# Kernel optimization log

Measured on AMD Instinct MI355X. Metric: run time of the kernel, lower is better.

## Reference

```python
import jax, jax.numpy as jnp
import numpy as np

EPS_ATTN = 1e-6
LN_EPS = 1e-5

def _layernorm(x, g, b):
    mu = jnp.mean(x, axis=-1, keepdims=True)
    var = jnp.var(x, axis=-1, keepdims=True)
    return (x - mu) * jax.lax.rsqrt(var + LN_EPS) * g + b

def _phi(x):
    return jax.nn.elu(x) + 1.0

def setup_inputs() -> dict:
    key = jax.random.key(0)
    ks = jax.random.split(key, 8)
    B, T, D, H = 2, 4096, 128, 128  # D = token_dim = d+1, H = hidden_dim
    s = 0.02
    return {
        "tokens": jax.random.normal(ks[0], (B, T, D), dtype=jnp.float32),
        "Wq": jax.random.normal(ks[1], (D, H), dtype=jnp.float32) * s,
        "Wk": jax.random.normal(ks[2], (D, H), dtype=jnp.float32) * s,
        "Wv": jax.random.normal(ks[3], (D, D), dtype=jnp.float32) * s,
        "Wg": jax.random.normal(ks[4], (D, D), dtype=jnp.float32) * s,
        "bg": jnp.zeros((D,), dtype=jnp.float32),
        "Wo": jax.random.normal(ks[5], (D, D), dtype=jnp.float32) * s,
        "g1": jnp.ones((D,), dtype=jnp.float32),
        "b1": jnp.zeros((D,), dtype=jnp.float32),
        "g2": jnp.ones((D,), dtype=jnp.float32),
        "b2": jnp.zeros((D,), dtype=jnp.float32),
    }

def reference(tokens, Wq, Wk, Wv, Wg, bg, Wo, g1, b1, g2, b2):
    x = _layernorm(tokens, g1, b1)                 # (b,t,m)
    Q = x @ Wq                                     # (b,t,h)
    K = x @ Wk                                     # (b,t,h)
    V = x @ Wv                                     # (b,t,m)
    G = jax.nn.sigmoid(x @ Wg + bg)                # (b,t,m)
    Vg = V * G
    Qp = _phi(Q)
    Kp = _phi(K)
    # causal linear attention via cumulative outer products
    kv = jnp.einsum('bth,btm->bthm', Kp, Vg)       # (b,t,h,m)
    S_kv = jnp.cumsum(kv, axis=1)
    S_k = jnp.cumsum(Kp, axis=1)
    numerator = jnp.einsum('bth,bthm->btm', Qp, S_kv)
    denom = jnp.maximum(jnp.einsum('bth,bth->bt', Qp, S_k), EPS_ATTN)
    attn_out = numerator / denom[..., None]
    out = tokens + (attn_out @ Wo) * 0.1
    return _layernorm(out, g2, b2)
```

## Files before the change

kernel.cpp:

```cpp
#include <hip/hip_runtime.h>
#include <math.h>

#define T_ 4096
#define D_ 128
#define NTOK 8192
#define CHUNK 64
#define NCB 64
#define NCH 128
#define LN_EPS 1e-5f
#define EPS_ATTN 1e-6f

typedef __attribute__((ext_vector_type(8))) short bf16x8;
typedef __attribute__((ext_vector_type(4))) short bf16x4;
typedef __attribute__((ext_vector_type(2))) short bf16x2;
typedef __attribute__((ext_vector_type(4))) float f32x4;

__device__ inline short f2bf(float f) {
  unsigned u = __builtin_bit_cast(unsigned, f);
  u += 0x7fffu + ((u >> 16) & 1u);
  return (short)(u >> 16);
}
__device__ inline float bf2f(short s) {
  unsigned u = ((unsigned)(unsigned short)s) << 16;
  return __builtin_bit_cast(float, u);
}
__device__ inline float phi_(float x) { return x > 0.f ? x + 1.f : __expf(x); }

__global__ __launch_bounds__(256) void k_wprep(const float* __restrict__ Wq,
    const float* __restrict__ Wk, const float* __restrict__ Wv,
    const float* __restrict__ Wg, const float* __restrict__ Wo,
    short* __restrict__ WT) {
  const float* W = blockIdx.x==0?Wq: blockIdx.x==1?Wk: blockIdx.x==2?Wv: blockIdx.x==3?Wg:Wo;
  short* out = WT + blockIdx.x*D_*D_;
  __shared__ float lds[128][132];
  const int tid = threadIdx.x;
  #pragma unroll
  for (int it = 0; it < 16; ++it) {
    const int f = it*1024 + tid*4;
    const int k = f >> 7, n = f & 127;
    const float4 v = *(const float4*)&W[f];
    lds[k][n] = v.x; lds[k][n+1] = v.y; lds[k][n+2] = v.z; lds[k][n+3] = v.w;
  }
  __syncthreads();
  #pragma unroll
  for (int it = 0; it < 16; ++it) {
    const int f = it*1024 + tid*4;
    const int n = f >> 7, k = f & 127;
    bf16x4 o;
    o.x = f2bf(lds[k][n]);   o.y = f2bf(lds[k+1][n]);
    o.z = f2bf(lds[k+2][n]); o.w = f2bf(lds[k+3][n]);
    *(bf16x4*)&out[f] = o;
  }
}

__global__ __launch_bounds__(256) void k_qkvg(const float* __restrict__ tokens,
    const short* __restrict__ WT,
    const float* __restrict__ g1, const float* __restrict__ b1,
    const float* __restrict__ bg,
    short* __restrict__ Qp, short* __restrict__ Kp, short* __restrict__ KpT,
    short* __restrict__ VgT) {
  const int m0 = blockIdx.x * 32;
  const int y = blockIdx.y;
  const int tid = threadIdx.x;
  const int w = tid >> 6, l = tid & 63;
  __shared__ short xs[32][136];
  __shared__ short wsd[128][136];

  {
    const float2 gg = *(const float2*)&g1[l*2];
    const float2 bb = *(const float2*)&b1[l*2];
    float2 tv[8];
    #pragma unroll
    for (int it = 0; it < 8; ++it)
      tv[it] = *(const float2*)&tokens[(m0 + w*8 + it)*D_ + l*2];
    #pragma unroll
    for (int it = 0; it < 8; ++it) {
      const float2 v = tv[it];
      float s = v.x + v.y, qq = v.x*v.x + v.y*v.y;
      #pragma unroll
      for (int off = 1; off < 64; off <<= 1) {
        s += __shfl_xor(s, off); qq += __shfl_xor(qq, off);
      }
      const float mean = s*(1.f/D_);
      const float r2 = rsqrtf(qq*(1.f/D_) - mean*mean + LN_EPS);
      bf16x2 o;
      o.x = f2bf((v.x-mean)*r2*gg.x + bb.x);
      o.y = f2bf((v.y-mean)*r2*gg.y + bb.y);
      *(bf16x2*)&xs[w*8 + it][l*2] = o;
    }
  }

  auto stageW = [&](const short* __restrict__ Wb) {
    for (int v = tid; v < 2048; v += 256) {
      const int n = v >> 4, c8 = (v & 15)*8;
      *(bf16x8*)&wsd[n][c8] = *(const bf16x8*)&Wb[n*D_ + c8];
    }
  };

  const int i = l & 15, q = l >> 4;
  auto gemm = [&](f32x4 (*acc)[2]) {
    #pragma unroll
    for (int kk = 0; kk < 4; ++kk) {
      bf16x8 a[2], bfr[2];
      #pragma unroll
      for (int mt = 0; mt < 2; ++mt) a[mt] = *(const bf16x8*)&xs[mt*16+i][kk*32+q*8];
      #pragma unroll
      for (int nt = 0; nt < 2; ++nt) bfr[nt] = *(const bf16x8*)&wsd[w*32+nt*16+i][kk*32+q*8];
      #pragma unroll
      for (int mt = 0; mt < 2; ++mt)
        #pragma unroll
        for (int nt = 0; nt < 2; ++nt)
          acc[mt][nt] = __builtin_amdgcn_mfma_f32_16x16x32_bf16(a[mt], bfr[nt], acc[mt][nt], 0, 0, 0);
    }
  };

  stageW(WT + (y == 2 ? 2 : y)*D_*D_);
  __syncthreads();
  f32x4 acc[2][2];
  #pragma unroll
  for (int mt = 0; mt < 2; ++mt)
    #pragma unroll
    for (int nt = 0; nt < 2; ++nt) acc[mt][nt] = (f32x4){0.f,0.f,0.f,0.f};
  gemm(acc);

  if (y == 0) {
    #pragma unroll
    for (int mt = 0; mt < 2; ++mt)
      #pragma unroll
      for (int nt = 0; nt < 2; ++nt) {
        const int h = w*32 + nt*16 + i;
        #pragma unroll
        for (int r = 0; r < 4; ++r)
          Qp[(m0 + mt*16 + 4*q + r)*D_ + h] = f2bf(phi_(acc[mt][nt][r]));
      }
  } else if (y == 1) {
    #pragma unroll
    for (int mt = 0; mt < 2; ++mt)
      #pragma unroll
      for (int nt = 0; nt < 2; ++nt) {
        const int h = w*32 + nt*16 + i;
        const int t0 = m0 + mt*16 + 4*q;
        bf16x4 o;
        #pragma unroll
        for (int r = 0; r < 4; ++r) {
          const short bv = f2bf(phi_(acc[mt][nt][r]));
          Kp[(t0+r)*D_ + h] = bv;
          o[r] = bv;
        }
        *(bf16x4*)&KpT[h*NTOK + t0] = o;
      }
  } else {
    __syncthreads();
    stageW(WT + 3*D_*D_);
    __syncthreads();
    f32x4 accg[2][2];
    #pragma unroll
    for (int mt = 0; mt < 2; ++mt)
      #pragma unroll
      for (int nt = 0; nt < 2; ++nt) accg[mt][nt] = (f32x4){0.f,0.f,0.f,0.f};
    gemm(accg);
    #pragma unroll
    for (int mt = 0; mt < 2; ++mt)
      #pragma unroll
      for (int nt = 0; nt < 2; ++nt) {
        const int h = w*32 + nt*16 + i;
        const int t0 = m0 + mt*16 + 4*q;
        const float bgd = bg[h];
        bf16x4 o;
        #pragma unroll
        for (int r = 0; r < 4; ++r) {
          const float gv = 1.f/(1.f + __expf(-(accg[mt][nt][r] + bgd)));
          o[r] = f2bf(acc[mt][nt][r] * gv);
        }
        *(bf16x4*)&VgT[h*NTOK + t0] = o;
      }
  }
}

__global__ __launch_bounds__(256) void k_chunkkv(const short* __restrict__ KpT,
    const short* __restrict__ VgT,
    float* __restrict__ KVT, float* __restrict__ Ksum) {
  const int c = blockIdx.x, hh = blockIdx.y, dh = blockIdx.z;
  const int tid = threadIdx.x;
  const int tb = c*CHUNK;
  __shared__ short vgl[64][72];
  __shared__ short kpl[64][72];
  __shared__ float ksp[64][5];
  for (int u = tid; u < 512; u += 256) {
    const int dd = u >> 3, c8 = (u & 7)*8;
    *(bf16x8*)&vgl[dd][c8] = *(const bf16x8*)&VgT[(dh*64+dd)*NTOK + tb + c8];
    *(bf16x8*)&kpl[dd][c8] = *(const bf16x8*)&KpT[(hh*64+dd)*NTOK + tb + c8];
  }
  __syncthreads();
  const int w = tid >> 6, l = tid & 63, i = l & 15, q = l >> 4;
  f32x4 acc[4];
  #pragma unroll
  for (int nt = 0; nt < 4; ++nt) acc[nt] = (f32x4){0.f,0.f,0.f,0.f};
  #pragma unroll
  for (int kk = 0; kk < 2; ++kk) {
    bf16x8 a = *(const bf16x8*)&vgl[w*16+i][kk*32+q*8];
    #pragma unroll
    for (int nt = 0; nt < 4; ++nt) {
      bf16x8 bb = *(const bf16x8*)&kpl[nt*16+i][kk*32+q*8];
      acc[nt] = __builtin_amdgcn_mfma_f32_16x16x32_bf16(a, bb, acc[nt], 0, 0, 0);
    }
  }
  float* KVc = KVT + (size_t)c*16384;
  #pragma unroll
  for (int nt = 0; nt < 4; ++nt)
    #pragma unroll
    for (int r = 0; r < 4; ++r) {
      const int d = dh*64 + w*16 + 4*q + r;
      const int h = hh*64 + nt*16 + i;
      KVc[d*D_ + h] = acc[nt][r];
    }
  if (dh == 0) {
    const int h = tid >> 2, part = tid & 3;
    float s = 0.f;
    #pragma unroll
    for (int t = 0; t < 16; ++t) s += bf2f(kpl[h][part*16 + t]);
    ksp[h][part] = s;
    __syncthreads();
    if (tid < 64)
      Ksum[c*D_ + hh*64 + tid] = ksp[tid][0]+ksp[tid][1]+ksp[tid][2]+ksp[tid][3];
  }
}

__global__ __launch_bounds__(256) void k_prescore(const float* __restrict__ KVT,
    short* __restrict__ KVTb, float* __restrict__ Ksum,
    const short* __restrict__ Qp, const short* __restrict__ Kp,
    short* __restrict__ A, float* __restrict__ rowsum) {
  const int tid = threadIdx.x;
  if (blockIdx.x < 128) {
    const int b = blockIdx.x >> 6;
    const int e = (blockIdx.x & 63)*256 + tid;
    const size_t base = (size_t)b*NCB*16384 + e;
    float run = 0.f;
    #pragma unroll 8
    for (int c = 0; c < NCB; ++c) {
      const float v = KVT[base + (size_t)c*16384];
      KVTb[base + (size_t)c*16384] = f2bf(run);
      run += v;
    }
    return;
  }
  if (blockIdx.x == 128) {
    const int b = tid >> 7, h = tid & 127;
    float run = 0.f;
    #pragma unroll 8
    for (int c = 0; c < NCB; ++c) {
      const int idx = (b*NCB + c)*128 + h;
      const float v = Ksum[idx];
      Ksum[idx] = run;
      run += v;
    }
    return;
  }
  const int c = blockIdx.x - 129;
  const int tb = c*CHUNK;
  __shared__ short qpl[64][136], kpl[64][136];
  #pragma unroll
  for (int u = tid; u < 1024; u += 256) {
    const int t = u >> 4, c8 = (u & 15)*8;
    *(bf16x8*)&qpl[t][c8] = *(const bf16x8*)&Qp[(tb+t)*D_ + c8];
    *(bf16x8*)&kpl[t][c8] = *(const bf16x8*)&Kp[(tb+t)*D_ + c8];
  }
  __syncthreads();
  const int w = tid >> 6, l = tid & 63, i = l & 15, q = l >> 4;
  f32x4 acc[4];
  #pragma unroll
  for (int nt = 0; nt < 4; ++nt) acc[nt] = (f32x4){0.f,0.f,0.f,0.f};
  #pragma unroll
  for (int kk = 0; kk < 4; ++kk) {
    bf16x8 a = *(const bf16x8*)&qpl[w*16+i][kk*32+q*8];
    for (int nt = 0; nt <= w; ++nt) {
      bf16x8 bb = *(const bf16x8*)&kpl[nt*16+i][kk*32+q*8];
      acc[nt] = __builtin_amdgcn_mfma_f32_16x16x32_bf16(a, bb, acc[nt], 0, 0, 0);
    }
  }
  short* Ac = A + c*4096;
  float rs[4] = {0.f,0.f,0.f,0.f};
  #pragma unroll
  for (int nt = 0; nt < 4; ++nt) {
    #pragma unroll
    for (int r = 0; r < 4; ++r) {
      const int t = w*16 + 4*q + r;
      const int s = nt*16 + i;
      const float v = (nt <= w && s <= t) ? acc[nt][r] : 0.f;
      rs[r] += v;
      Ac[t*64 + s] = f2bf(v);
    }
  }
  #pragma unroll
  for (int r = 0; r < 4; ++r) {
    #pragma unroll
    for (int off = 1; off < 16; off <<= 1) rs[r] += __shfl_xor(rs[r], off);
  }
  if (i == 0) {
    #pragma unroll
    for (int r = 0; r < 4; ++r) rowsum[c*64 + w*16 + 4*q + r] = rs[r];
  }
}

__global__ __launch_bounds__(256) void k_attnout(const short* __restrict__ Aintra,
    const short* __restrict__ Qp, const short* __restrict__ VgT,
    const short* __restrict__ KVTb, const float* __restrict__ Ksum,
    const float* __restrict__ rowsum, short* __restrict__ attn) {
  const int c = blockIdx.x, dq = blockIdx.y, tid = threadIdx.x;
  const int tb = c*CHUNK;
  __shared__ short at[64][200], bt[32][200];
  __shared__ float ksl[128], dpart[64][4], denl[64];
  const short* Ac = Aintra + c*4096;
  #pragma unroll
  for (int u = tid; u < 512; u += 256) {
    const int t = u >> 3, c8 = (u & 7)*8;
    *(bf16x8*)&at[t][c8] = *(const bf16x8*)&Ac[t*64 + c8];
  }
  #pragma unroll
  for (int u = tid; u < 1024; u += 256) {
    const int t = u >> 4, c8 = (u & 15)*8;
    *(bf16x8*)&at[t][64 + c8] = *(const bf16x8*)&Qp[(tb+t)*D_ + c8];
  }
  for (int u = tid; u < 256; u += 256) {
    const int dd = u >> 3, c8 = (u & 7)*8;
    *(bf16x8*)&bt[dd][c8] = *(const bf16x8*)&VgT[(dq*32+dd)*NTOK + tb + c8];
  }
  #pragma unroll
  for (int u = tid; u < 512; u += 256) {
    const int dd = u >> 4, c8 = (u & 15)*8;
    *(bf16x8*)&bt[dd][64 + c8] = *(const bf16x8*)&KVTb[(size_t)c*16384 + (dq*32+dd)*D_ + c8];
  }
  if (tid < 128) ksl[tid] = Ksum[c*128 + tid];
  __syncthreads();
  {
    const int t = tid >> 2, part = tid & 3;
    float dot = 0.f;
    #pragma unroll
    for (int h = 0; h < 32; ++h) dot += bf2f(at[t][64 + part*32 + h]) * ksl[part*32 + h];
    dpart[t][part] = dot;
  }
  __syncthreads();
  if (tid < 64)
    denl[tid] = fmaxf(rowsum[c*64 + tid] + dpart[tid][0]+dpart[tid][1]+dpart[tid][2]+dpart[tid][3], EPS_ATTN);
  __syncthreads();
  const int w = tid >> 6, l = tid & 63, i = l & 15, q = l >> 4;
  f32x4 acc[2];
  #pragma unroll
  for (int nt = 0; nt < 2; ++nt) acc[nt] = (f32x4){0.f,0.f,0.f,0.f};
  #pragma unroll
  for (int kk = 0; kk < 6; ++kk) {
    bf16x8 a = *(const bf16x8*)&at[w*16+i][kk*32+q*8];
    #pragma unroll
    for (int nt = 0; nt < 2; ++nt) {
      bf16x8 bb = *(const bf16x8*)&bt[nt*16+i][kk*32+q*8];
      acc[nt] = __builtin_amdgcn_mfma_f32_16x16x32_bf16(a, bb, acc[nt], 0, 0, 0);
    }
  }
  #pragma unroll
  for (int r = 0; r < 4; ++r) {
    const int t = w*16 + 4*q + r;
    const float inv = 1.f / denl[t];
    #pragma unroll
    for (int nt = 0; nt < 2; ++nt)
      attn[(size_t)(tb+t)*D_ + dq*32 + nt*16 + i] = f2bf(acc[nt][r] * inv);
  }
}

__global__ __launch_bounds__(256) void k_outln2(const short* __restrict__ attn,
    const short* __restrict__ WoT, const float* __restrict__ tokens,
    const float* __restrict__ g2, const float* __restrict__ b2,
    float* __restrict__ out) {
  const int m0 = blockIdx.x*16, tid = threadIdx.x;
  __shared__ short al[16][136], wl[128][136];
  __shared__ float tl[16][132];
  __shared__ float suml[16][4], ssql[16][4];
  __shared__ float meanl[16], rstdl[16];
  __shared__ float gl[128], bl2[128];
  for (int u = tid; u < 256; u += 256) {
    const int t = u >> 4, c8 = (u & 15)*8;
    *(bf16x8*)&al[t][c8] = *(const bf16x8*)&attn[(m0+t)*D_ + c8];
  }
  #pragma unroll
  for (int u = tid; u < 2048; u += 256) {
    const int n = u >> 4, c8 = (u & 15)*8;
    *(bf16x8*)&wl[n][c8] = *(const bf16x8*)&WoT[n*D_ + c8];
  }
  #pragma unroll
  for (int u = tid; u < 512; u += 256) {
    const int t = u >> 5, c4 = (u & 31)*4;
    *(float4*)&tl[t][c4] = *(const float4*)&tokens[(m0+t)*D_ + c4];
  }
  if (tid < 128) { gl[tid] = g2[tid]; bl2[tid] = b2[tid]; }
  __syncthreads();
  const int w = tid >> 6, l = tid & 63, i = l & 15, q = l >> 4;
  f32x4 acc[2];
  #pragma unroll
  for (int j = 0; j < 2; ++j) acc[j] = (f32x4){0.f,0.f,0.f,0.f};
  #pragma unroll
  for (int kk = 0; kk < 4; ++kk) {
    bf16x8 a = *(const bf16x8*)&al[i][kk*32+q*8];
    #pragma unroll
    for (int j = 0; j < 2; ++j) {
      bf16x8 bb = *(const bf16x8*)&wl[(w*2+j)*16+i][kk*32+q*8];
      acc[j] = __builtin_amdgcn_mfma_f32_16x16x32_bf16(a, bb, acc[j], 0, 0, 0);
    }
  }
  float p[4][2], ps[4], qs[4];
  #pragma unroll
  for (int r = 0; r < 4; ++r) {
    const int t = 4*q + r;
    ps[r] = 0.f; qs[r] = 0.f;
    #pragma unroll
    for (int j = 0; j < 2; ++j) {
      const int col = w*32 + j*16 + i;
      const float v = tl[t][col] + 0.1f*acc[j][r];
      p[r][j] = v; ps[r] += v; qs[r] += v*v;
    }
  }
  #pragma unroll
  for (int r = 0; r < 4; ++r) {
    #pragma unroll
    for (int off = 1; off < 16; off <<= 1) {
      ps[r] += __shfl_xor(ps[r], off);
      qs[r] += __shfl_xor(qs[r], off);
    }
  }
  if (i == 0) {
    #pragma unroll
    for (int r = 0; r < 4; ++r) {
      suml[4*q+r][w] = ps[r];
      ssql[4*q+r][w] = qs[r];
    }
  }
  __syncthreads();
  if (tid < 16) {
    const float s = suml[tid][0]+suml[tid][1]+suml[tid][2]+suml[tid][3];
    const float qq = ssql[tid][0]+ssql[tid][1]+ssql[tid][2]+ssql[tid][3];
    const float mean = s*(1.f/D_);
    meanl[tid] = mean;
    rstdl[tid] = rsqrtf(qq*(1.f/D_) - mean*mean + LN_EPS);
  }
  __syncthreads();
  #pragma unroll
  for (int r = 0; r < 4; ++r) {
    const int t = 4*q + r;
    const float mean = meanl[t], rr = rstdl[t];
    #pragma unroll
    for (int j = 0; j < 2; ++j) {
      const int col = w*32 + j*16 + i;
      out[(m0+t)*D_ + col] = (p[r][j]-mean)*rr*gl[col] + bl2[col];
    }
  }
}

extern "C" void kernel_launch(void* const* d_in, const int* in_sizes, int n_in,
                              void* d_out, int out_size, void* d_ws, size_t ws_size,
                              hipStream_t stream) {
  const float* tokens = (const float*)d_in[0];
  const float* Wq = (const float*)d_in[1];
  const float* Wk = (const float*)d_in[2];
  const float* Wv = (const float*)d_in[3];
  const float* Wg = (const float*)d_in[4];
  const float* bg = (const float*)d_in[5];
  const float* Wo = (const float*)d_in[6];
  const float* g1 = (const float*)d_in[7];
  const float* b1 = (const float*)d_in[8];
  const float* g2 = (const float*)d_in[9];
  const float* b2 = (const float*)d_in[10];

  char* base = (char*)d_ws;
  short* Qp     = (short*)(base);
  short* Kp     = (short*)(base + (2u<<20));
  short* KpT    = (short*)(base + (4u<<20));
  short* VgT    = (short*)(base + (6u<<20));
  short* attn   = (short*)(base + (8u<<20));
  short* KVTb   = (short*)(base + (10u<<20));
  short* Aintra = (short*)(base + (14u<<20));
  short* WT     = (short*)(base + (15u<<20));
  float* rowsum = (float*)(base + (15u<<20) + (256u<<10));
  float* Ksum   = (float*)(base + (15u<<20) + (512u<<10));
  float* KVT    = (float*)(base + (16u<<20));

  short* WoT = WT + 4*D_*D_;

  k_wprep<<<5, 256, 0, stream>>>(Wq, Wk, Wv, Wg, Wo, WT);
  k_qkvg<<<dim3(NTOK/32, 3), 256, 0, stream>>>(tokens, WT, g1, b1, bg,
                                               Qp, Kp, KpT, VgT);
  k_chunkkv<<<dim3(NCH, 2, 2), 256, 0, stream>>>(KpT, VgT, KVT, Ksum);
  k_prescore<<<257, 256, 0, stream>>>(KVT, KVTb, Ksum, Qp, Kp, Aintra, rowsum);
  k_attnout<<<dim3(NCH, 4), 256, 0, stream>>>(Aintra, Qp, VgT, KVTb, Ksum, rowsum, attn);
  k_outln2<<<NTOK/16, 256, 0, stream>>>(attn, WoT, tokens, g2, b2, (float*)d_out);
}
```

Before: 114.5 us.

## Fuse all stages into one cooperative persistent kernel with grid syncs

Replaces the six separate kernel launches with a single cooperative kernel of 512 blocks that separates the stages with grid-wide syncs. The aim is to remove launch gaps and per-kernel ramp-up and tail costs. Work is also rebalanced across blocks: weight prep is split over 10 blocks, Q and K blocks each handle two row tiles, and the score and chunk-KV stages share one phase. The risks are the cost of the grid barriers and lower occupancy from the large static shared-memory buffer and the 2-blocks-per-CU launch bound.

Result: slower. 413.6 us (+261.3%).

```diff
diff --git a/kernel.cpp b/kernel.cpp
--- a/kernel.cpp
+++ b/kernel.cpp
@@ -1,7 +1,9 @@
 #include <hip/hip_runtime.h>
+#include <hip/hip_cooperative_groups.h>
 #include <math.h>
 
-#define T_ 4096
+namespace cg = cooperative_groups;
+
 #define D_ 128
 #define NTOK 8192
 #define CHUNK 64
@@ -9,6 +11,7 @@
 #define NCH 128
 #define LN_EPS 1e-5f
 #define EPS_ATTN 1e-6f
+#define NBLK 512
 
 typedef __attribute__((ext_vector_type(8))) short bf16x8;
 typedef __attribute__((ext_vector_type(4))) short bf16x4;
@@ -26,430 +29,477 @@
 }
 __device__ inline float phi_(float x) { return x > 0.f ? x + 1.f : __expf(x); }
 
-__global__ __launch_bounds__(256) void k_wprep(const float* __restrict__ Wq,
-    const float* __restrict__ Wk, const float* __restrict__ Wv,
-    const float* __restrict__ Wg, const float* __restrict__ Wo,
-    short* __restrict__ WT) {
-  const float* W = blockIdx.x==0?Wq: blockIdx.x==1?Wk: blockIdx.x==2?Wv: blockIdx.x==3?Wg:Wo;
-  short* out = WT + blockIdx.x*D_*D_;
-  __shared__ float lds[128][132];
+__global__ __launch_bounds__(256, 2) void k_mega(
+    const float* __restrict__ tokens,
+    const float* __restrict__ Wq, const float* __restrict__ Wk,
+    const float* __restrict__ Wv, const float* __restrict__ Wg,
+    const float* __restrict__ bgp, const float* __restrict__ Wo,
+    const float* __restrict__ g1, const float* __restrict__ b1,
+    const float* __restrict__ g2, const float* __restrict__ b2,
+    float* __restrict__ out, char* __restrict__ ws)
+{
+  cg::grid_group grid = cg::this_grid();
   const int tid = threadIdx.x;
-  #pragma unroll
-  for (int it = 0; it < 16; ++it) {
-    const int f = it*1024 + tid*4;
-    const int k = f >> 7, n = f & 127;
-    const float4 v = *(const float4*)&W[f];
-    lds[k][n] = v.x; lds[k][n+1] = v.y; lds[k][n+2] = v.z; lds[k][n+3] = v.w;
+  const int bid = blockIdx.x;
+
+  short* Qp     = (short*)(ws);
+  short* Kp     = (short*)(ws + (2u<<20));
+  short* KpT    = (short*)(ws + (4u<<20));
+  short* VgT    = (short*)(ws + (6u<<20));
+  short* attnb  = (short*)(ws + (8u<<20));
+  short* KVTb   = (short*)(ws + (10u<<20));
+  short* Aintra = (short*)(ws + (14u<<20));
+  short* WT     = (short*)(ws + (15u<<20));
+  float* rowsum = (float*)(ws + (15u<<20) + (256u<<10));
+  float* Ksum   = (float*)(ws + (15u<<20) + (512u<<10));
+  float* KVT    = (float*)(ws + (16u<<20));
+
+  __shared__ __align__(16) char smem[62720];
+
+  const int w = tid >> 6, l = tid & 63;
+  const int i = l & 15, q = l >> 4;
+
+  if (bid < 10) {
+    const int mat = bid >> 1, half = bid & 1;
+    const float* W = mat==0?Wq: mat==1?Wk: mat==2?Wv: mat==3?Wg:Wo;
+    short* o = WT + mat*D_*D_;
+    float (*lds)[132] = (float(*)[132])smem;
+    #pragma unroll
+    for (int it = 0; it < 8; ++it) {
+      const int f = it*1024 + tid*4;
+      const int kk = f >> 7, n = f & 127;
+      const float4 v = *(const float4*)&W[(half*64 + kk)*D_ + n];
+      lds[kk][n] = v.x; lds[kk][n+1] = v.y; lds[kk][n+2] = v.z; lds[kk][n+3] = v.w;
+    }
+    __syncthreads();
+    #pragma unroll
+    for (int it = 0; it < 8; ++it) {
+      const int f = it*1024 + tid*4;
+      const int n = f >> 6, kl = f & 63;
+      bf16x4 ov;
+      ov.x = f2bf(lds[kl][n]);   ov.y = f2bf(lds[kl+1][n]);
+      ov.z = f2bf(lds[kl+2][n]); ov.w = f2bf(lds[kl+3][n]);
+      *(bf16x4*)&o[n*D_ + half*64 + kl] = ov;
+    }
   }
-  __syncthreads();
-  #pragma unroll
-  for (int it = 0; it < 16; ++it) {
-    const int f = it*1024 + tid*4;
-    const int n = f >> 7, k = f & 127;
-    bf16x4 o;
-    o.x = f2bf(lds[k][n]);   o.y = f2bf(lds[k+1][n]);
-    o.z = f2bf(lds[k+2][n]); o.w = f2bf(lds[k+3][n]);
-    *(bf16x4*)&out[f] = o;
+  grid.sync();
+
+  {
+    short (*xs)[136]  = (short(*)[136])smem;
+    short (*wsd)[136] = (short(*)[136])(smem + 8704);
+
+    auto stageW = [&](const short* __restrict__ Wb) {
+      for (int v = tid; v < 2048; v += 256) {
+        const int n = v >> 4, c8 = (v & 15)*8;
+        *(bf16x8*)&wsd[n][c8] = *(const bf16x8*)&Wb[n*D_ + c8];
+      }
+    };
+    auto doLN = [&](int m0) {
+      const float2 gg = *(const float2*)&g1[l*2];
+      const float2 bb = *(const float2*)&b1[l*2];
+      float2 tv[8];
+      #pragma unroll
+      for (int it = 0; it < 8; ++it)
+        tv[it] = *(const float2*)&tokens[(m0 + w*8 + it)*D_ + l*2];
+      #pragma unroll
+      for (int it = 0; it < 8; ++it) {
+        const float2 v = tv[it];
+        float s = v.x + v.y, qq = v.x*v.x + v.y*v.y;
+        #pragma unroll
+        for (int off = 1; off < 64; off <<= 1) {
+          s += __shfl_xor(s, off); qq += __shfl_xor(qq, off);
+        }
+        const float mean = s*(1.f/D_);
+        const float r2 = rsqrtf(qq*(1.f/D_) - mean*mean + LN_EPS);
+        bf16x2 o;
+        o.x = f2bf((v.x-mean)*r2*gg.x + bb.x);
+        o.y = f2bf((v.y-mean)*r2*gg.y + bb.y);
+        *(bf16x2*)&xs[w*8 + it][l*2] = o;
+      }
+    };
+    auto gemm = [&](f32x4 (*acc)[2]) {
+      #pragma unroll
+      for (int kk = 0; kk < 4; ++kk) {
+        bf16x8 a[2], bfr[2];
+        #pragma unroll
+        for (int mt = 0; mt < 2; ++mt) a[mt] = *(const bf16x8*)&xs[mt*16+i][kk*32+q*8];
+        #pragma unroll
+        for (int nt = 0; nt < 2; ++nt) bfr[nt] = *(const bf16x8*)&wsd[w*32+nt*16+i][kk*32+q*8];
+        #pragma unroll
+        for (int mt = 0; mt < 2; ++mt)
+          #pragma unroll
+          for (int nt = 0; nt < 2; ++nt)
+            acc[mt][nt] = __builtin_amdgcn_mfma_f32_16x16x32_bf16(a[mt], bfr[nt], acc[mt][nt], 0, 0, 0);
+      }
+    };
+
+    if (bid < 256) {
+      const int m0 = bid * 32;
+      doLN(m0);
+      stageW(WT + 2*D_*D_);
+      __syncthreads();
+      f32x4 acc[2][2], accg[2][2];
+      #pragma unroll
+      for (int mt = 0; mt < 2; ++mt)
+        #pragma unroll
+        for (int nt = 0; nt < 2; ++nt) acc[mt][nt] = (f32x4){0.f,0.f,0.f,0.f};
+      gemm(acc);
+      __syncthreads();
+      stageW(WT + 3*D_*D_);
+      __syncthreads();
+      #pragma unroll
+      for (int mt = 0; mt < 2; ++mt)
+        #pragma unroll
+        for (int nt = 0; nt < 2; ++nt) accg[mt][nt] = (f32x4){0.f,0.f,0.f,0.f};
+      gemm(accg);
+      #pragma unroll
+      for (int mt = 0; mt < 2; ++mt)
+        #pragma unroll
+        for (int nt = 0; nt < 2; ++nt) {
+          const int h = w*32 + nt*16 + i;
+          const int t0 = m0 + mt*16 + 4*q;
+          const float bgd = bgp[h];
+          bf16x4 o;
+          #pragma unroll
+          for (int r = 0; r < 4; ++r) {
+            const float gv = 1.f/(1.f + __expf(-(accg[mt][nt][r] + bgd)));
+            o[r] = f2bf(acc[mt][nt][r] * gv);
+          }
+          *(bf16x4*)&VgT[h*NTOK + t0] = o;
+        }
+    } else if (bid < 384) {
+      stageW(WT);
+      for (int uu = 0; uu < 2; ++uu) {
+        const int m0 = ((bid - 256)*2 + uu) * 32;
+        __syncthreads();
+        doLN(m0);
+        __syncthreads();
+        f32x4 acc[2][2];
+        #pragma unroll
+        for (int mt = 0; mt < 2; ++mt)
+          #pragma unroll
+          for (int nt = 0; nt < 2; ++nt) acc[mt][nt] = (f32x4){0.f,0.f,0.f,0.f};
+        gemm(acc);
+        #pragma unroll
+        for (int mt = 0; mt < 2; ++mt)
+          #pragma unroll
+          for (int nt = 0; nt < 2; ++nt) {
+            const int h = w*32 + nt*16 + i;
+            #pragma unroll
+            for (int r = 0; r < 4; ++r)
+              Qp[(m0 + mt*16 + 4*q + r)*D_ + h] = f2bf(phi_(acc[mt][nt][r]));
+          }
+      }
+    } else {
+      stageW(WT + D_*D_);
+      for (int uu = 0; uu < 2; ++uu) {
+        const int m0 = ((bid - 384)*2 + uu) * 32;
+        __syncthreads();
+        doLN(m0);
+        __syncthreads();
+        f32x4 acc[2][2];
+        #pragma unroll
+        for (int mt = 0; mt < 2; ++mt)
+          #pragma unroll
+          for (int nt = 0; nt < 2; ++nt) acc[mt][nt] = (f32x4){0.f,0.f,0.f,0.f};
+        gemm(acc);
+        #pragma unroll
+        for (int mt = 0; mt < 2; ++mt)
+          #pragma unroll
+          for (int nt = 0; nt < 2; ++nt) {
+            const int h = w*32 + nt*16 + i;
+            const int t0 = m0 + mt*16 + 4*q;
+            bf16x4 o;
+            #pragma unroll
+            for (int r = 0; r < 4; ++r) {
+              const short bv = f2bf(phi_(acc[mt][nt][r]));
+              Kp[(t0+r)*D_ + h] = bv;
+              o[r] = bv;
+            }
+            *(bf16x4*)&KpT[h*NTOK + t0] = o;
+          }
+      }
+    }
   }
-}
-
-__global__ __launch_bounds__(256) void k_qkvg(const float* __restrict__ tokens,
-    const short* __restrict__ WT,
-    const float* __restrict__ g1, const float* __restrict__ b1,
-    const float* __restrict__ bg,
-    short* __restrict__ Qp, short* __restrict__ Kp, short* __restrict__ KpT,
-    short* __restrict__ VgT) {
-  const int m0 = blockIdx.x * 32;
-  const int y = blockIdx.y;
-  const int tid = threadIdx.x;
-  const int w = tid >> 6, l = tid & 63;
-  __shared__ short xs[32][136];
-  __shared__ short wsd[128][136];
+  grid.sync();
 
   {
-    const float2 gg = *(const float2*)&g1[l*2];
-    const float2 bb = *(const float2*)&b1[l*2];
-    float2 tv[8];
-    #pragma unroll
-    for (int it = 0; it < 8; ++it)
-      tv[it] = *(const float2*)&tokens[(m0 + w*8 + it)*D_ + l*2];
-    #pragma unroll
-    for (int it = 0; it < 8; ++it) {
-      const float2 v = tv[it];
-      float s = v.x + v.y, qq = v.x*v.x + v.y*v.y;
-      #pragma unroll
-      for (int off = 1; off < 64; off <<= 1) {
-        s += __shfl_xor(s, off); qq += __shfl_xor(qq, off);
-      }
-      const float mean = s*(1.f/D_);
-      const float r2 = rsqrtf(qq*(1.f/D_) - mean*mean + LN_EPS);
-      bf16x2 o;
-      o.x = f2bf((v.x-mean)*r2*gg.x + bb.x);
-      o.y = f2bf((v.y-mean)*r2*gg.y + bb.y);
-      *(bf16x2*)&xs[w*8 + it][l*2] = o;
+    auto chunkkv = [&](int v) {
+      const int c = v & 127, hh = (v >> 7) & 1, dh = v >> 8;
+      const int tb = c*CHUNK;
+      short (*vgl)[72] = (short(*)[72])smem;
+      short (*kpl)[72] = (short(*)[72])(smem + 9216);
+      float (*ksp)[5]  = (float(*)[5])(smem + 18432);
+      for (int u = tid; u < 512; u += 256) {
+        const int dd = u >> 3, c8 = (u & 7)*8;
+        *(bf16x8*)&vgl[dd][c8] = *(const bf16x8*)&VgT[(dh*64+dd)*NTOK + tb + c8];
+        *(bf16x8*)&kpl[dd][c8] = *(const bf16x8*)&KpT[(hh*64+dd)*NTOK + tb + c8];
+      }
+      __syncthreads();
+      f32x4 acc[4];
+      #pragma unroll
+      for (int nt = 0; nt < 4; ++nt) acc[nt] = (f32x4){0.f,0.f,0.f,0.f};
+      #pragma unroll
+      for (int kk = 0; kk < 2; ++kk) {
+        bf16x8 a = *(const bf16x8*)&vgl[w*16+i][kk*32+q*8];
+        #pragma unroll
+        for (int nt = 0; nt < 4; ++nt) {
+          bf16x8 bb = *(const bf16x8*)&kpl[nt*16+i][kk*32+q*8];
+          acc[nt] = __builtin_amdgcn_mfma_f32_16x16x32_bf16(a, bb, acc[nt], 0, 0, 0);
+        }
+      }
+      float* KVc = KVT + (size_t)c*16384;
+      #pragma unroll
+      for (int nt = 0; nt < 4; ++nt)
+        #pragma unroll
+        for (int r = 0; r < 4; ++r) {
+          const int d = dh*64 + w*16 + 4*q + r;
+          const int h = hh*64 + nt*16 + i;
+          KVc[d*D_ + h] = acc[nt][r];
+        }
+      if (dh == 0) {
+        const int hq = tid >> 2, part = tid & 3;
+        float s = 0.f;
+        #pragma unroll
+        for (int t = 0; t < 16; ++t) s += bf2f(kpl[hq][part*16 + t]);
+        ksp[hq][part] = s;
+        __syncthreads();
+        if (tid < 64)
+          Ksum[c*D_ + hh*64 + tid] = ksp[tid][0]+ksp[tid][1]+ksp[tid][2]+ksp[tid][3];
+      }
+    };
+
+    auto scores = [&](int c) {
+      const int tb = c*CHUNK;
+      short (*qpl)[136] = (short(*)[136])smem;
+      short (*kpl)[136] = (short(*)[136])(smem + 17408);
+      for (int u = tid; u < 1024; u += 256) {
+        const int t = u >> 4, c8 = (u & 15)*8;
+        *(bf16x8*)&qpl[t][c8] = *(const bf16x8*)&Qp[(tb+t)*D_ + c8];
+        *(bf16x8*)&kpl[t][c8] = *(const bf16x8*)&Kp[(tb+t)*D_ + c8];
+      }
+      __syncthreads();
+      f32x4 acc[4];
+      #pragma unroll
+      for (int nt = 0; nt < 4; ++nt) acc[nt] = (f32x4){0.f,0.f,0.f,0.f};
+      #pragma unroll
+      for (int kk = 0; kk < 4; ++kk) {
+        bf16x8 a = *(const bf16x8*)&qpl[w*16+i][kk*32+q*8];
+        #pragma unroll
+        for (int nt = 0; nt < 4; ++nt) {
+          if (nt <= w) {
+            bf16x8 bb = *(const bf16x8*)&kpl[nt*16+i][kk*32+q*8];
+            acc[nt] = __builtin_amdgcn_mfma_f32_16x16x32_bf16(a, bb, acc[nt], 0, 0, 0);
+          }
+        }
+      }
+      short* Ac = Aintra + c*4096;
+      float rs[4] = {0.f,0.f,0.f,0.f};
+      #pragma unroll
+      for (int nt = 0; nt < 4; ++nt) {
+        #pragma unroll
+        for (int r = 0; r < 4; ++r) {
+          const int t = w*16 + 4*q + r;
+          const int s = nt*16 + i;
+          const float v = (nt <= w && s <= t) ? acc[nt][r] : 0.f;
+          rs[r] += v;
+          Ac[t*64 + s] = f2bf(v);
+        }
+      }
+      #pragma unroll
+      for (int r = 0; r < 4; ++r) {
+        #pragma unroll
+        for (int off = 1; off < 16; off <<= 1) rs[r] += __shfl_xor(rs[r], off);
+      }
+      if (i == 0) {
+        #pragma unroll
+        for (int r = 0; r < 4; ++r) rowsum[c*64 + w*16 + 4*q + r] = rs[r];
+      }
+    };
+
+    if (bid < 128) {
+      scores(bid);
+      __syncthreads();
+      chunkkv(384 + bid);
+    } else {
+      chunkkv(bid - 128);
     }
   }
-
-  auto stageW = [&](const short* __restrict__ Wb) {
-    for (int v = tid; v < 2048; v += 256) {
-      const int n = v >> 4, c8 = (v & 15)*8;
-      *(bf16x8*)&wsd[n][c8] = *(const bf16x8*)&Wb[n*D_ + c8];
-    }
-  };
-
-  const int i = l & 15, q = l >> 4;
-  auto gemm = [&](f32x4 (*acc)[2]) {
-    #pragma unroll
-    for (int kk = 0; kk < 4; ++kk) {
-      bf16x8 a[2], bfr[2];
-      #pragma unroll
-      for (int mt = 0; mt < 2; ++mt) a[mt] = *(const bf16x8*)&xs[mt*16+i][kk*32+q*8];
-      #pragma unroll
-      for (int nt = 0; nt < 2; ++nt) bfr[nt] = *(const bf16x8*)&wsd[w*32+nt*16+i][kk*32+q*8];
-      #pragma unroll
-      for (int mt = 0; mt < 2; ++mt)
-        #pragma unroll
-        for (int nt = 0; nt < 2; ++nt)
-          acc[mt][nt] = __builtin_amdgcn_mfma_f32_16x16x32_bf16(a[mt], bfr[nt], acc[mt][nt], 0, 0, 0);
-    }
-  };
-
-  stageW(WT + (y == 2 ? 2 : y)*D_*D_);
-  __syncthreads();
-  f32x4 acc[2][2];
-  #pragma unroll
-  for (int mt = 0; mt < 2; ++mt)
-    #pragma unroll
-    for (int nt = 0; nt < 2; ++nt) acc[mt][nt] = (f32x4){0.f,0.f,0.f,0.f};
-  gemm(acc);
-
-  if (y == 0) {
-    #pragma unroll
-    for (int mt = 0; mt < 2; ++mt)
+  grid.sync();
+
+  {
+    if (bid < 128) {
+      const int b = bid >> 6;
+      const int e = (bid & 63)*256 + tid;
+      const size_t basei = (size_t)b*NCB*16384 + e;
+      float run = 0.f;
+      #pragma unroll 8
+      for (int c = 0; c < NCB; ++c) {
+        const float v = KVT[basei + (size_t)c*16384];
+        KVTb[basei + (size_t)c*16384] = f2bf(run);
+        run += v;
+      }
+    } else if (bid == 128) {
+      const int b = tid >> 7, h = tid & 127;
+      float run = 0.f;
+      #pragma unroll 8
+      for (int c = 0; c < NCB; ++c) {
+        const int idx = (b*NCB + c)*128 + h;
+        const float v = Ksum[idx];
+        Ksum[idx] = run;
+        run += v;
+      }
+    }
+  }
+  grid.sync();
+
+  {
+    const int c = bid & 127, dq = bid >> 7;
+    const int tb = c*CHUNK;
+    short (*at)[200] = (short(*)[200])smem;
+    short (*bt)[200] = (short(*)[200])(smem + 25600);
+    float* ksl        = (float*)(smem + 38400);
+    float (*dpart)[4] = (float(*)[4])(smem + 38912);
+    float* denl       = (float*)(smem + 39936);
+    const short* Ac = Aintra + c*4096;
+    for (int u = tid; u < 512; u += 256) {
+      const int t = u >> 3, c8 = (u & 7)*8;
+      *(bf16x8*)&at[t][c8] = *(const bf16x8*)&Ac[t*64 + c8];
+    }
+    for (int u = tid; u < 1024; u += 256) {
+      const int t = u >> 4, c8 = (u & 15)*8;
+      *(bf16x8*)&at[t][64 + c8] = *(const bf16x8*)&Qp[(tb+t)*D_ + c8];
+    }
+    for (int u = tid; u < 256; u += 256) {
+      const int dd = u >> 3, c8 = (u & 7)*8;
+      *(bf16x8*)&bt[dd][c8] = *(const bf16x8*)&VgT[(dq*32+dd)*NTOK + tb + c8];
+    }
+    for (int u = tid; u < 512; u += 256) {
+      const int dd = u >> 4, c8 = (u & 15)*8;
+      *(bf16x8*)&bt[dd][64 + c8] = *(const bf16x8*)&KVTb[(size_t)c*16384 + (dq*32+dd)*D_ + c8];
+    }
+    if (tid < 128) ksl[tid] = Ksum[c*128 + tid];
+    __syncthreads();
+    {
+      const int t = tid >> 2, part = tid & 3;
+      float dot = 0.f;
+      #pragma unroll
+      for (int h = 0; h < 32; ++h) dot += bf2f(at[t][64 + part*32 + h]) * ksl[part*32 + h];
+      dpart[t][part] = dot;
+    }
+    __syncthreads();
+    if (tid < 64)
+      denl[tid] = fmaxf(rowsum[c*64 + tid] + dpart[tid][0]+dpart[tid][1]+dpart[tid][2]+dpart[tid][3], EPS_ATTN);
+    __syncthreads();
+    f32x4 acc[2];
+    #pragma unroll
+    for (int nt = 0; nt < 2; ++nt) acc[nt] = (f32x4){0.f,0.f,0.f,0.f};
+    #pragma unroll
+    for (int kk = 0; kk < 6; ++kk) {
+      bf16x8 a = *(const bf16x8*)&at[w*16+i][kk*32+q*8];
       #pragma unroll
       for (int nt = 0; nt < 2; ++nt) {
-        const int h = w*32 + nt*16 + i;
-        #pragma unroll
-        for (int r = 0; r < 4; ++r)
-          Qp[(m0 + mt*16 + 4*q + r)*D_ + h] = f2bf(phi_(acc[mt][nt][r]));
-      }
-  } else if (y == 1) {
-    #pragma unroll
-    for (int mt = 0; mt < 2; ++mt)
-      #pragma unroll
-      for (int nt = 0; nt < 2; ++nt) {
-        const int h = w*32 + nt*16 + i;
-        const int t0 = m0 + mt*16 + 4*q;
-        bf16x4 o;
-        #pragma unroll
-        for (int r = 0; r < 4; ++r) {
-          const short bv = f2bf(phi_(acc[mt][nt][r]));
-          Kp[(t0+r)*D_ + h] = bv;
-          o[r] = bv;
-        }
-        *(bf16x4*)&KpT[h*NTOK + t0] = o;
-      }
-  } else {
-    __syncthreads();
-    stageW(WT + 3*D_*D_);
-    __syncthreads();
-    f32x4 accg[2][2];
-    #pragma unroll
-    for (int mt = 0; mt < 2; ++mt)
-      #pragma unroll
-      for (int nt = 0; nt < 2; ++nt) accg[mt][nt] = (f32x4){0.f,0.f,0.f,0.f};
-    gemm(accg);
-    #pragma unroll
-    for (int mt = 0; mt < 2; ++mt)
-      #pragma unroll
-      for (int nt = 0; nt < 2; ++nt) {
-        const int h = w*32 + nt*16 + i;
-        const int t0 = m0 + mt*16 + 4*q;
-        const float bgd = bg[h];
-        bf16x4 o;
-        #pragma unroll
-        for (int r = 0; r < 4; ++r) {
-          const float gv = 1.f/(1.f + __expf(-(accg[mt][nt][r] + bgd)));
-          o[r] = f2bf(acc[mt][nt][r] * gv);
-        }
-        *(bf16x4*)&VgT[h*NTOK + t0] = o;
-      }
-  }
-}
-
-__global__ __launch_bounds__(256) void k_chunkkv(const short* __restrict__ KpT,
-    const short* __restrict__ VgT,
-    float* __restrict__ KVT, float* __restrict__ Ksum) {
-  const int c = blockIdx.x, hh = blockIdx.y, dh = blockIdx.z;
-  const int tid = threadIdx.x;
-  const int tb = c*CHUNK;
-  __shared__ short vgl[64][72];
-  __shared__ short kpl[64][72];
-  __shared__ float ksp[64][5];
-  for (int u = tid; u < 512; u += 256) {
-    const int dd = u >> 3, c8 = (u & 7)*8;
-    *(bf16x8*)&vgl[dd][c8] = *(const bf16x8*)&VgT[(dh*64+dd)*NTOK + tb + c8];
-    *(bf16x8*)&kpl[dd][c8] = *(const bf16x8*)&KpT[(hh*64+dd)*NTOK + tb + c8];
-  }
-  __syncthreads();
-  const int w = tid >> 6, l = tid & 63, i = l & 15, q = l >> 4;
-  f32x4 acc[4];
-  #pragma unroll
-  for (int nt = 0; nt < 4; ++nt) acc[nt] = (f32x4){0.f,0.f,0.f,0.f};
-  #pragma unroll
-  for (int kk = 0; kk < 2; ++kk) {
-    bf16x8 a = *(const bf16x8*)&vgl[w*16+i][kk*32+q*8];
-    #pragma unroll
-    for (int nt = 0; nt < 4; ++nt) {
-      bf16x8 bb = *(const bf16x8*)&kpl[nt*16+i][kk*32+q*8];
-      acc[nt] = __builtin_amdgcn_mfma_f32_16x16x32_bf16(a, bb, acc[nt], 0, 0, 0);
-    }
-  }
-  float* KVc = KVT + (size_t)c*16384;
-  #pragma unroll
-  for (int nt = 0; nt < 4; ++nt)
-    #pragma unroll
-    for (int r = 0; r < 4; ++r) {
-      const int d = dh*64 + w*16 + 4*q + r;
-      const int h = hh*64 + nt*16 + i;
-      KVc[d*D_ + h] = acc[nt][r];
-    }
-  if (dh == 0) {
-    const int h = tid >> 2, part = tid & 3;
-    float s = 0.f;
-    #pragma unroll
-    for (int t = 0; t < 16; ++t) s += bf2f(kpl[h][part*16 + t]);
-    ksp[h][part] = s;
-    __syncthreads();
-    if (tid < 64)
-      Ksum[c*D_ + hh*64 + tid] = ksp[tid][0]+ksp[tid][1]+ksp[tid][2]+ksp[tid][3];
-  }
-}
-
-__global__ __launch_bounds__(256) void k_prescore(const float* __restrict__ KVT,
-    short* __restrict__ KVTb, float* __restrict__ Ksum,
-    const short* __restrict__ Qp, const short* __restrict__ Kp,
-    short* __restrict__ A, float* __restrict__ rowsum) {
-  const int tid = threadIdx.x;
-  if (blockIdx.x < 128) {
-    const int b = blockIdx.x >> 6;
-    const int e = (blockIdx.x & 63)*256 + tid;
-    const size_t base = (size_t)b*NCB*16384 + e;
-    float run = 0.f;
-    #pragma unroll 8
-    for (int c = 0; c < NCB; ++c) {
-      const float v = KVT[base + (size_t)c*16384];
-      KVTb[base + (size_t)c*16384] = f2bf(run);
-      run += v;
-    }
-    return;
-  }
-  if (blockIdx.x == 128) {
-    const int b = tid >> 7, h = tid & 127;
-    float run = 0.f;
-    #pragma unroll 8
-    for (int c = 0; c < NCB; ++c) {
-      const int idx = (b*NCB + c)*128 + h;
-      const float v = Ksum[idx];
-      Ksum[idx] = run;
-      run += v;
-    }
-    return;
-  }
-  const int c = blockIdx.x - 129;
-  const int tb = c*CHUNK;
-  __shared__ short qpl[64][136], kpl[64][136];
-  #pragma unroll
-  for (int u = tid; u < 1024; u += 256) {
-    const int t = u >> 4, c8 = (u & 15)*8;
-    *(bf16x8*)&qpl[t][c8] = *(const bf16x8*)&Qp[(tb+t)*D_ + c8];
-    *(bf16x8*)&kpl[t][c8] = *(const bf16x8*)&Kp[(tb+t)*D_ + c8];
-  }
-  __syncthreads();
-  const int w = tid >> 6, l = tid & 63, i = l & 15, q = l >> 4;
-  f32x4 acc[4];
-  #pragma unroll
-  for (int nt = 0; nt < 4; ++nt) acc[nt] = (f32x4){0.f,0.f,0.f,0.f};
-  #pragma unroll
-  for (int kk = 0; kk < 4; ++kk) {
-    bf16x8 a = *(const bf16x8*)&qpl[w*16+i][kk*32+q*8];
-    for (int nt = 0; nt <= w; ++nt) {
-      bf16x8 bb = *(const bf16x8*)&kpl[nt*16+i][kk*32+q*8];
-      acc[nt] = __builtin_amdgcn_mfma_f32_16x16x32_bf16(a, bb, acc[nt], 0, 0, 0);
-    }
-  }
-  short* Ac = A + c*4096;
-  float rs[4] = {0.f,0.f,0.f,0.f};
-  #pragma unroll
-  for (int nt = 0; nt < 4; ++nt) {
+        bf16x8 bb = *(const bf16x8*)&bt[nt*16+i][kk*32+q*8];
+        acc[nt] = __builtin_amdgcn_mfma_f32_16x16x32_bf16(a, bb, acc[nt], 0, 0, 0);
+      }
+    }
     #pragma unroll
     for (int r = 0; r < 4; ++r) {
       const int t = w*16 + 4*q + r;
-      const int s = nt*16 + i;
-      const float v = (nt <= w && s <= t) ? acc[nt][r] : 0.f;
-      rs[r] += v;
-      Ac[t*64 + s] = f2bf(v);
+      const float inv = 1.f / denl[t];
+      #pragma unroll
+      for (int nt = 0; nt < 2; ++nt)
+        attnb[(size_t)(tb+t)*D_ + dq*32 + nt*16 + i] = f2bf(acc[nt][r] * inv);
     }
   }
-  #pragma unroll
-  for (int r = 0; r < 4; ++r) {
-    #pragma unroll
-    for (int off = 1; off < 16; off <<= 1) rs[r] += __shfl_xor(rs[r], off);
-  }
-  if (i == 0) {
-    #pragma unroll
-    for (int r = 0; r < 4; ++r) rowsum[c*64 + w*16 + 4*q + r] = rs[r];
-  }
-}
-
-__global__ __launch_bounds__(256) void k_attnout(const short* __restrict__ Aintra,
-    const short* __restrict__ Qp, const short* __restrict__ VgT,
-    const short* __restrict__ KVTb, const float* __restrict__ Ksum,
-    const float* __restrict__ rowsum, short* __restrict__ attn) {
-  const int c = blockIdx.x, dq = blockIdx.y, tid = threadIdx.x;
-  const int tb = c*CHUNK;
-  __shared__ short at[64][200], bt[32][200];
-  __shared__ float ksl[128], dpart[64][4], denl[64];
-  const short* Ac = Aintra + c*4096;
-  #pragma unroll
-  for (int u = tid; u < 512; u += 256) {
-    const int t = u >> 3, c8 = (u & 7)*8;
-    *(bf16x8*)&at[t][c8] = *(const bf16x8*)&Ac[t*64 + c8];
-  }
-  #pragma unroll
-  for (int u = tid; u < 1024; u += 256) {
-    const int t = u >> 4, c8 = (u & 15)*8;
-    *(bf16x8*)&at[t][64 + c8] = *(const bf16x8*)&Qp[(tb+t)*D_ + c8];
-  }
-  for (int u = tid; u < 256; u += 256) {
-    const int dd = u >> 3, c8 = (u & 7)*8;
-    *(bf16x8*)&bt[dd][c8] = *(const bf16x8*)&VgT[(dq*32+dd)*NTOK + tb + c8];
-  }
-  #pragma unroll
-  for (int u = tid; u < 512; u += 256) {
-    const int dd = u >> 4, c8 = (u & 15)*8;
-    *(bf16x8*)&bt[dd][64 + c8] = *(const bf16x8*)&KVTb[(size_t)c*16384 + (dq*32+dd)*D_ + c8];
-  }
-  if (tid < 128) ksl[tid] = Ksum[c*128 + tid];
-  __syncthreads();
-  {
-    const int t = tid >> 2, part = tid & 3;
-    float dot = 0.f;
-    #pragma unroll
-    for (int h = 0; h < 32; ++h) dot += bf2f(at[t][64 + part*32 + h]) * ksl[part*32 + h];
-    dpart[t][part] = dot;
-  }
-  __syncthreads();
-  if (tid < 64)
-    denl[tid] = fmaxf(rowsum[c*64 + tid] + dpart[tid][0]+dpart[tid][1]+dpart[tid][2]+dpart[tid][3], EPS_ATTN);
-  __syncthreads();
-  const int w = tid >> 6, l = tid & 63, i = l & 15, q = l >> 4;
-  f32x4 acc[2];
-  #pragma unroll
-  for (int nt = 0; nt < 2; ++nt) acc[nt] = (f32x4){0.f,0.f,0.f,0.f};
-  #pragma unroll
-  for (int kk = 0; kk < 6; ++kk) {
-    bf16x8 a = *(const bf16x8*)&at[w*16+i][kk*32+q*8];
-    #pragma unroll
-    for (int nt = 0; nt < 2; ++nt) {
-      bf16x8 bb = *(const bf16x8*)&bt[nt*16+i][kk*32+q*8];
-      acc[nt] = __builtin_amdgcn_mfma_f32_16x16x32_bf16(a, bb, acc[nt], 0, 0, 0);
-    }
-  }
-  #pragma unroll
-  for (int r = 0; r < 4; ++r) {
-    const int t = w*16 + 4*q + r;
-    const float inv = 1.f / denl[t];
-    #pragma unroll
-    for (int nt = 0; nt < 2; ++nt)
-      attn[(size_t)(tb+t)*D_ + dq*32 + nt*16 + i] = f2bf(acc[nt][r] * inv);
-  }
-}
-
-__global__ __launch_bounds__(256) void k_outln2(const short* __restrict__ attn,
-    const short* __restrict__ WoT, const float* __restrict__ tokens,
-    const float* __restrict__ g2, const float* __restrict__ b2,
-    float* __restrict__ out) {
-  const int m0 = blockIdx.x*16, tid = threadIdx.x;
-  __shared__ short al[16][136], wl[128][136];
-  __shared__ float tl[16][132];
-  __shared__ float suml[16][4], ssql[16][4];
-  __shared__ float meanl[16], rstdl[16];
-  __shared__ float gl[128], bl2[128];
-  for (int u = tid; u < 256; u += 256) {
-    const int t = u >> 4, c8 = (u & 15)*8;
-    *(bf16x8*)&al[t][c8] = *(const bf16x8*)&attn[(m0+t)*D_ + c8];
-  }
-  #pragma unroll
-  for (int u = tid; u < 2048; u += 256) {
-    const int n = u >> 4, c8 = (u & 15)*8;
-    *(bf16x8*)&wl[n][c8] = *(const bf16x8*)&WoT[n*D_ + c8];
-  }
-  #pragma unroll
-  for (int u = tid; u < 512; u += 256) {
-    const int t = u >> 5, c4 = (u & 31)*4;
-    *(float4*)&tl[t][c4] = *(const float4*)&tokens[(m0+t)*D_ + c4];
-  }
-  if (tid < 128) { gl[tid] = g2[tid]; bl2[tid] = b2[tid]; }
-  __syncthreads();
-  const int w = tid >> 6, l = tid & 63, i = l & 15, q = l >> 4;
-  f32x4 acc[2];
-  #pragma unroll
-  for (int j = 0; j < 2; ++j) acc[j] = (f32x4){0.f,0.f,0.f,0.f};
-  #pragma unroll
-  for (int kk = 0; kk < 4; ++kk) {
-    bf16x8 a = *(const bf16x8*)&al[i][kk*32+q*8];
-    #pragma unroll
-    for (int j = 0; j < 2; ++j) {
-      bf16x8 bb = *(const bf16x8*)&wl[(w*2+j)*16+i][kk*32+q*8];
-      acc[j] = __builtin_amdgcn_mfma_f32_16x16x32_bf16(a, bb, acc[j], 0, 0, 0);
-    }
-  }
-  float p[4][2], ps[4], qs[4];
-  #pragma unroll
-  for (int r = 0; r < 4; ++r) {
-    const int t = 4*q + r;
-    ps[r] = 0.f; qs[r] = 0.f;
-    #pragma unroll
-    for (int j = 0; j < 2; ++j) {
-      const int col = w*32 + j*16 + i;
-      const float v = tl[t][col] + 0.1f*acc[j][r];
-      p[r][j] = v; ps[r] += v; qs[r] += v*v;
-    }
-  }
-  #pragma unroll
-  for (int r = 0; r < 4; ++r) {
-    #pragma unroll
-    for (int off = 1; off < 16; off <<= 1) {
-      ps[r] += __shfl_xor(ps[r], off);
-      qs[r] += __shfl_xor(qs[r], off);
-    }
-  }
-  if (i == 0) {
-    #pragma unroll
-    for (int r = 0; r < 4; ++r) {
-      suml[4*q+r][w] = ps[r];
-      ssql[4*q+r][w] = qs[r];
-    }
-  }
-  __syncthreads();
-  if (tid < 16) {
-    const float s = suml[tid][0]+suml[tid][1]+suml[tid][2]+suml[tid][3];
-    const float qq = ssql[tid][0]+ssql[tid][1]+ssql[tid][2]+ssql[tid][3];
-    const float mean = s*(1.f/D_);
-    meanl[tid] = mean;
-    rstdl[tid] = rsqrtf(qq*(1.f/D_) - mean*mean + LN_EPS);
-  }
-  __syncthreads();
-  #pragma unroll
-  for (int r = 0; r < 4; ++r) {
-    const int t = 4*q + r;
-    const float mean = meanl[t], rr = rstdl[t];
-    #pragma unroll
-    for (int j = 0; j < 2; ++j) {
-      const int col = w*32 + j*16 + i;
-      out[(m0+t)*D_ + col] = (p[r][j]-mean)*rr*gl[col] + bl2[col];
-    }
+  grid.sync();
+
+  if (bid < 256) {
+    const int m0 = bid * 32;
+    short (*al)[136] = (short(*)[136])smem;
+    short (*wl)[136] = (short(*)[136])(smem + 8704);
+    float (*tl)[132] = (float(*)[132])(smem + 43520);
+    float (*suml)[4] = (float(*)[4])(smem + 60416);
+    float (*ssql)[4] = (float(*)[4])(smem + 60928);
+    float* meanl = (float*)(smem + 61440);
+    float* rstdl = (float*)(smem + 61568);
+    float* gl    = (float*)(smem + 61696);
+    float* bl2   = (float*)(smem + 62208);
+    const short* WoT = WT + 4*D_*D_;
+
+    for (int u = tid; u < 512; u += 256) {
+      const int t = u >> 4, c8 = (u & 15)*8;
+      *(bf16x8*)&al[t][c8] = *(const bf16x8*)&attnb[(m0+t)*D_ + c8];
+    }
+    for (int u = tid; u < 2048; u += 256) {
+      const int n = u >> 4, c8 = (u & 15)*8;
+      *(bf16x8*)&wl[n][c8] = *(const bf16x8*)&WoT[n*D_ + c8];
+    }
+    for (int u = tid; u < 1024; u += 256) {
+      const int t = u >> 5, c4 = (u & 31)*4;
+      *(float4*)&tl[t][c4] = *(const float4*)&tokens[(m0+t)*D_ + c4];
+    }
+    if (tid < 128) { gl[tid] = g2[tid]; bl2[tid] = b2[tid]; }
+    __syncthreads();
+
+    f32x4 acc[2][2];
+    #pragma unroll
+    for (int mt = 0; mt < 2; ++mt)
+      #pragma unroll
+      for (int j = 0; j < 2; ++j) acc[mt][j] = (f32x4){0.f,0.f,0.f,0.f};
+    #pragma unroll
+    for (int kk = 0; kk < 4; ++kk) {
+      bf16x8 a[2];
+      #pragma unroll
+      for (int mt = 0; mt < 2; ++mt) a[mt] = *(const bf16x8*)&al[mt*16+i][kk*32+q*8];
+      #pragma unroll
+      for (int j = 0; j < 2; ++j) {
+        bf16x8 bb = *(const bf16x8*)&wl[(w*2+j)*16+i][kk*32+q*8];
+        #pragma unroll
+        for (int mt = 0; mt < 2; ++mt)
+          acc[mt][j] = __builtin_amdgcn_mfma_f32_16x16x32_bf16(a[mt], bb, acc[mt][j], 0, 0, 0);
+      }
+    }
+    float p[2][4][2];
+    #pragma unroll
+    for (int mt = 0; mt < 2; ++mt)
+      #pragma unroll
+      for (int r = 0; r < 4; ++r) {
+        const int t = mt*16 + 4*q + r;
+        float ps = 0.f, qs = 0.f;
+        #pragma unroll
+        for (int j = 0; j < 2; ++j) {
+          const int col = w*32 + j*16 + i;
+          const float v = tl[t][col] + 0.1f*acc[mt][j][r];
+          p[mt][r][j] = v; ps += v; qs += v*v;
+        }
+        #pragma unroll
+        for (int off = 1; off < 16; off <<= 1) {
+          ps += __shfl_xor(ps, off); qs += __shfl_xor(qs, off);
+        }
+        if (i == 0) { suml[t][w] = ps; ssql[t][w] = qs; }
+      }
+    __syncthreads();
+    if (tid < 32) {
+      const float s = suml[tid][0]+suml[tid][1]+suml[tid][2]+suml[tid][3];
+      const float qq = ssql[tid][0]+ssql[tid][1]+ssql[tid][2]+ssql[tid][3];
+      const float mean = s*(1.f/D_);
+      meanl[tid] = mean;
+      rstdl[tid] = rsqrtf(qq*(1.f/D_) - mean*mean + LN_EPS);
+    }
+    __syncthreads();
+    #pragma unroll
+    for (int mt = 0; mt < 2; ++mt)
+      #pragma unroll
+      for (int r = 0; r < 4; ++r) {
+        const int t = mt*16 + 4*q + r;
+        const float mean = meanl[t], rr = rstdl[t];
+        #pragma unroll
+        for (int j = 0; j < 2; ++j) {
+          const int col = w*32 + j*16 + i;
+          out[(m0+t)*D_ + col] = (p[mt][r][j]-mean)*rr*gl[col] + bl2[col];
+        }
+      }
   }
 }
 
@@ -467,27 +517,11 @@
   const float* b1 = (const float*)d_in[8];
   const float* g2 = (const float*)d_in[9];
   const float* b2 = (const float*)d_in[10];
-
-  char* base = (char*)d_ws;
-  short* Qp     = (short*)(base);
-  short* Kp     = (short*)(base + (2u<<20));
-  short* KpT    = (short*)(base + (4u<<20));
-  short* VgT    = (short*)(base + (6u<<20));
-  short* attn   = (short*)(base + (8u<<20));
-  short* KVTb   = (short*)(base + (10u<<20));
-  short* Aintra = (short*)(base + (14u<<20));
-  short* WT     = (short*)(base + (15u<<20));
-  float* rowsum = (float*)(base + (15u<<20) + (256u<<10));
-  float* Ksum   = (float*)(base + (15u<<20) + (512u<<10));
-  float* KVT    = (float*)(base + (16u<<20));
-
-  short* WoT = WT + 4*D_*D_;
-
-  k_wprep<<<5, 256, 0, stream>>>(Wq, Wk, Wv, Wg, Wo, WT);
-  k_qkvg<<<dim3(NTOK/32, 3), 256, 0, stream>>>(tokens, WT, g1, b1, bg,
-                                               Qp, Kp, KpT, VgT);
-  k_chunkkv<<<dim3(NCH, 2, 2), 256, 0, stream>>>(KpT, VgT, KVT, Ksum);
-  k_prescore<<<257, 256, 0, stream>>>(KVT, KVTb, Ksum, Qp, Kp, Aintra, rowsum);
-  k_attnout<<<dim3(NCH, 4), 256, 0, stream>>>(Aintra, Qp, VgT, KVTb, Ksum, rowsum, attn);
-  k_outln2<<<NTOK/16, 256, 0, stream>>>(attn, WoT, tokens, g2, b2, (float*)d_out);
+  float* outp = (float*)d_out;
+  char* wsp = (char*)d_ws;
+
+  void* args[] = { (void*)&tokens, (void*)&Wq, (void*)&Wk, (void*)&Wv, (void*)&Wg,
+                   (void*)&bg, (void*)&Wo, (void*)&g1, (void*)&b1, (void*)&g2,
+                   (void*)&b2, (void*)&outp, (void*)&wsp };
+  hipLaunchCooperativeKernel((const void*)k_mega, dim3(NBLK), dim3(256), args, 0, stream);
 }
```
